# Kernel optimization log

Measured on AMD Instinct MI355X. Metric: run time of the kernel, lower is better.

The kernel has to match this reference:

```python
import jax, jax.numpy as jnp
import numpy as np

B, N1, N2, C1, C2, MLP_OUT = 16, 4096, 1024, 128, 256, 256


def setup_inputs() -> dict:
    key = jax.random.key(0)
    k = jax.random.split(key, 8)
    xyz1 = jax.random.normal(k[0], (B, N1, 3), dtype=jnp.float32)
    feat1 = jax.random.normal(k[1], (B, N1, C1), dtype=jnp.float32)
    xyz2 = jax.random.normal(k[2], (B, N2, 3), dtype=jnp.float32)
    feat2 = jax.random.normal(k[3], (B, N2, C2), dtype=jnp.float32)
    d_in = C1 + C2
    W1 = jax.random.normal(k[4], (d_in, MLP_OUT), dtype=jnp.float32) / np.sqrt(d_in)
    b1 = jnp.zeros((MLP_OUT,), dtype=jnp.float32)
    W2 = jax.random.normal(k[5], (MLP_OUT, MLP_OUT), dtype=jnp.float32) / np.sqrt(MLP_OUT)
    b2 = jnp.zeros((MLP_OUT,), dtype=jnp.float32)
    return {"xyz1": xyz1, "feat1": feat1, "xyz2": xyz2, "feat2": feat2,
            "W1": W1, "b1": b1, "W2": W2, "b2": b2}


def reference(xyz1, feat1, xyz2, feat2, W1, b1, W2, b2):
    # squared pairwise distances [B, N1, N2]
    dists = jnp.sum((xyz1[:, :, None, :] - xyz2[:, None, :, :]) ** 2, axis=-1)
    # 3 nearest neighbors (smallest distances)
    neg_d3, idx = jax.lax.top_k(-dists, 3)      # [B, N1, 3]
    d3 = jnp.maximum(-neg_d3, 1e-10)
    w = 1.0 / d3
    w = w / jnp.sum(w, axis=-1, keepdims=True)   # [B, N1, 3]
    # gather neighbor features: [B, N1, 3, C2]
    neighbor_feats = jax.vmap(lambda f, i: f[i])(feat2, idx)
    interpolated = jnp.sum(w[..., None] * neighbor_feats, axis=2)  # [B, N1, C2]
    new_feat = jnp.concatenate([interpolated, feat1], axis=-1)     # [B, N1, C2+C1]
    h = jax.nn.relu(new_feat @ W1 + b1)
    return jax.nn.relu(h @ W2 + b2)
```

## Files before the change

kernel.cpp:

```cpp
#include <hip/hip_runtime.h>
#include <cstdint>
#include <cstddef>

typedef unsigned short ushort_t;
typedef unsigned int uint_t;

typedef __bf16 bf16x8 __attribute__((ext_vector_type(8)));
typedef float floatx4 __attribute__((ext_vector_type(4)));

#define B_ 16
#define N1_ 4096
#define N2_ 1024
#define C1_ 128
#define C2_ 256
#define DIN_ 384
#define DOUT_ 256
#define M_ (B_ * N1_)


__device__ __forceinline__ ushort_t f2bf(float f) {
  unsigned int u = __builtin_bit_cast(unsigned int, f);
  u = (u + 0x7fffu + ((u >> 16) & 1u)) >> 16;
  return (ushort_t)u;
}


__global__ __launch_bounds__(256) void prep_kernel(
    const float* __restrict__ W1, const float* __restrict__ W2,
    ushort_t* __restrict__ W1s, ushort_t* __restrict__ W2s) {
  int e = blockIdx.x * 256 + threadIdx.x;
  if (e < DOUT_ * DIN_) {
    int kk = e & 31, n = (e >> 5) & 255, t = e >> 13;
    W1s[e] = f2bf(W1[(size_t)(t * 32 + kk) * DOUT_ + n]);
  }
  if (e < DOUT_ * DOUT_) {
    int kk = e & 31, n = (e >> 5) & 255, t = e >> 13;
    W2s[e] = f2bf(W2[(size_t)(t * 32 + kk) * DOUT_ + n]);
  }
}


__device__ __forceinline__ void ins_exact(float& s0, float& s1, float& s2,
                                          int& i0, int& i1, int& i2,
                                          float d, int p) {
  float ns2 = __builtin_amdgcn_fmed3f(d, s1, s2);
  float ns1 = __builtin_amdgcn_fmed3f(d, s0, s1);
  float ns0 = fminf(d, s0);
  bool c0 = d < s0, c1 = d < s1, c2 = d < s2;
  i2 = c1 ? i1 : (c2 ? p : i2);
  i1 = c0 ? i0 : (c1 ? p : i1);
  i0 = c0 ? p : i0;
  s0 = ns0; s1 = ns1; s2 = ns2;
}

__device__ __forceinline__ void ins_merge(float& s0, float& s1, float& s2,
                                          int& i0, int& i1, int& i2,
                                          float e, int j) {
  bool t0 = (e < s0) || (e == s0 && j < i0);
  bool t1 = (e < s1) || (e == s1 && j < i1);
  bool t2 = (e < s2) || (e == s2 && j < i2);
  s2 = t1 ? s1 : (t2 ? e : s2);
  i2 = t1 ? i1 : (t2 ? j : i2);
  s1 = t0 ? s0 : (t1 ? e : s1);
  i1 = t0 ? i0 : (t1 ? j : i1);
  s0 = t0 ? e : s0;
  i0 = t0 ? j : i0;
}


__global__ __launch_bounds__(256, 2) void fused_kernel(
    const float* __restrict__ xyz1, const float* __restrict__ xyz2,
    const float* __restrict__ feat1, const float* __restrict__ feat2,
    const ushort_t* __restrict__ W1s, const float* __restrict__ b1,
    const ushort_t* __restrict__ W2s, const float* __restrict__ b2,
    float* __restrict__ out) {
  __shared__ __align__(16) ushort_t As[32 * 384];
  __shared__ int idxL[32 * 3];
  __shared__ float wL[32 * 3];

  const int tid = threadIdx.x;
  const int wave = tid >> 6;
  const int lane = tid & 63;
  const int m = lane & 15;
  const int q = lane >> 4;
  const int row0 = blockIdx.x * 32;
  const int b = row0 >> 12;

  float4* xs4 = (float4*)As;
  {
    const float4* p24 = (const float4*)(xyz2 + (size_t)b * (N2_ * 3));
    float4 A = p24[3 * tid + 0];
    float4 Bv = p24[3 * tid + 1];
    float4 Cv = p24[3 * tid + 2];
    xs4[4 * tid + 0] = make_float4(A.x, A.y, A.z, 0.0f);
    xs4[4 * tid + 1] = make_float4(A.w, Bv.x, Bv.y, 0.0f);
    xs4[4 * tid + 2] = make_float4(Bv.z, Bv.w, Cv.x, 0.0f);
    xs4[4 * tid + 3] = make_float4(Cv.y, Cv.z, Cv.w, 0.0f);
  }
  __syncthreads();

  {
    const int g = tid >> 3;
    const int sub = tid & 7;
    const int row = row0 + g;
    const float* p1 = xyz1 + (size_t)row * 3;
    float x1 = p1[0], y1 = p1[1], z1 = p1[2];

    float s0 = 3.0e38f, s1 = 3.0e38f, s2 = 3.0e38f;
    int i0 = 0, i1 = 0, i2 = 0;

    int p = sub;
#pragma unroll 8
    for (int t = 0; t < N2_ / 8; ++t) {
      float4 qv = xs4[p];
      float dx = x1 - qv.x;
      float dy = y1 - qv.y;
      float dz = z1 - qv.z;
      float d = dx * dx + dy * dy + dz * dz;
      ins_exact(s0, s1, s2, i0, i1, i2, d, p);
      p += 8;
    }

#pragma unroll
    for (int mm = 1; mm <= 4; mm <<= 1) {
      float e0 = __shfl_xor(s0, mm), e1 = __shfl_xor(s1, mm), e2 = __shfl_xor(s2, mm);
      int j0 = __shfl_xor(i0, mm), j1 = __shfl_xor(i1, mm), j2 = __shfl_xor(i2, mm);
      ins_merge(s0, s1, s2, i0, i1, i2, e0, j0);
      ins_merge(s0, s1, s2, i0, i1, i2, e1, j1);
      ins_merge(s0, s1, s2, i0, i1, i2, e2, j2);
    }

    if (sub == 0) {
      float r0 = 1.0f / fmaxf(s0, 1e-10f);
      float r1 = 1.0f / fmaxf(s1, 1e-10f);
      float r2 = 1.0f / fmaxf(s2, 1e-10f);
      float s = 1.0f / (r0 + r1 + r2);
      idxL[g * 3 + 0] = i0;
      idxL[g * 3 + 1] = i1;
      idxL[g * 3 + 2] = i2;
      wL[g * 3 + 0] = r0 * s;
      wL[g * 3 + 1] = r1 * s;
      wL[g * 3 + 2] = r2 * s;
    }
  }
  __syncthreads();

#pragma unroll 4
  for (int it = 0; it < 8; ++it) {
    int rl = wave * 8 + it;
    int row = row0 + rl;
    int i0 = idxL[rl * 3 + 0], i1 = idxL[rl * 3 + 1], i2 = idxL[rl * 3 + 2];
    float w0 = wL[rl * 3 + 0], w1 = wL[rl * 3 + 1], w2 = wL[rl * 3 + 2];

    const float4* f0 = (const float4*)(feat2 + ((size_t)b * N2_ + i0) * C2_);
    const float4* f1 = (const float4*)(feat2 + ((size_t)b * N2_ + i1) * C2_);
    const float4* f2 = (const float4*)(feat2 + ((size_t)b * N2_ + i2) * C2_);
    float4 a = f0[lane];
    float4 c = f1[lane];
    float4 d = f2[lane];
    float vx = w0 * a.x + w1 * c.x + w2 * d.x;
    float vy = w0 * a.y + w1 * c.y + w2 * d.y;
    float vz = w0 * a.z + w1 * c.z + w2 * d.z;
    float vw = w0 * a.w + w1 * c.w + w2 * d.w;
    uint_t lo = (uint_t)f2bf(vx) | ((uint_t)f2bf(vy) << 16);
    uint_t hi = (uint_t)f2bf(vz) | ((uint_t)f2bf(vw) << 16);
    int e = (lane >> 3) * 1024 + rl * 32 + ((4 * lane) & 31);
    *(uint2*)&As[e] = make_uint2(lo, hi);

    float2 t1 = ((const float2*)(feat1 + (size_t)row * C1_))[lane];
    uint_t pk = (uint_t)f2bf(t1.x) | ((uint_t)f2bf(t1.y) << 16);
    int e1 = (8 + (lane >> 4)) * 1024 + rl * 32 + ((2 * lane) & 31);
    *(uint_t*)&As[e1] = pk;
  }
  __syncthreads();

  const int b_off = (wave * 64 + m) * 32 + q * 8;
  const int a_base = m * 32 + q * 8;

  floatx4 acc[2][4];
#pragma unroll
  for (int i = 0; i < 2; ++i)
#pragma unroll
    for (int j = 0; j < 4; ++j) acc[i][j] = (floatx4)0.0f;

  {
    bf16x8 bf0[4], bf1[4], af[2];
#pragma unroll
    for (int j = 0; j < 4; ++j)
      bf0[j] = *(const bf16x8*)(W1s + b_off + j * 512);
#pragma unroll
    for (int t = 0; t < 12; t += 2) {
#pragma unroll
      for (int j = 0; j < 4; ++j)
        bf1[j] = *(const bf16x8*)(W1s + (size_t)(t + 1) * 8192 + b_off + j * 512);
#pragma unroll
      for (int i = 0; i < 2; ++i)
        af[i] = *(const bf16x8*)&As[t * 1024 + a_base + i * 512];
#pragma unroll
      for (int i = 0; i < 2; ++i)
#pragma unroll
        for (int j = 0; j < 4; ++j)
          acc[i][j] = __builtin_amdgcn_mfma_f32_16x16x32_bf16(af[i], bf0[j],
                                                              acc[i][j], 0, 0, 0);
      if (t + 2 < 12) {
#pragma unroll
        for (int j = 0; j < 4; ++j)
          bf0[j] = *(const bf16x8*)(W1s + (size_t)(t + 2) * 8192 + b_off + j * 512);
      }
#pragma unroll
      for (int i = 0; i < 2; ++i)
        af[i] = *(const bf16x8*)&As[(t + 1) * 1024 + a_base + i * 512];
#pragma unroll
      for (int i = 0; i < 2; ++i)
#pragma unroll
        for (int j = 0; j < 4; ++j)
          acc[i][j] = __builtin_amdgcn_mfma_f32_16x16x32_bf16(af[i], bf1[j],
                                                              acc[i][j], 0, 0, 0);
    }
  }
  __syncthreads();

  ushort_t* HS = As;
#pragma unroll
  for (int j = 0; j < 4; ++j) {
    int col = wave * 64 + j * 16 + m;
    float bv = b1[col];
    int cb = (col >> 3) & 3;
    int tb = (col >> 5) * 1024 + (col & 7);
#pragma unroll
    for (int i = 0; i < 2; ++i)
#pragma unroll
      for (int r = 0; r < 4; ++r) {
        int row = i * 16 + q * 4 + r;
        float v = acc[i][j][r] + bv;
        v = v > 0.0f ? v : 0.0f;
        int ch = cb ^ ((row >> 2) & 3);
        HS[tb + row * 32 + ch * 8] = f2bf(v);
      }
  }
  __syncthreads();

  floatx4 acc2[2][4];
#pragma unroll
  for (int i = 0; i < 2; ++i)
#pragma unroll
    for (int j = 0; j < 4; ++j) acc2[i][j] = (floatx4)0.0f;

  {
    bf16x8 bf0[4], bf1[4], af[2];
#pragma unroll
    for (int j = 0; j < 4; ++j)
      bf0[j] = *(const bf16x8*)(W2s + b_off + j * 512);
#pragma unroll
    for (int t = 0; t < 8; t += 2) {
#pragma unroll
      for (int j = 0; j < 4; ++j)
        bf1[j] = *(const bf16x8*)(W2s + (size_t)(t + 1) * 8192 + b_off + j * 512);
#pragma unroll
      for (int i = 0; i < 2; ++i) {
        int row = m + 16 * i;
        int ch = q ^ ((row >> 2) & 3);
        af[i] = *(const bf16x8*)&HS[t * 1024 + row * 32 + ch * 8];
      }
#pragma unroll
      for (int i = 0; i < 2; ++i)
#pragma unroll
        for (int j = 0; j < 4; ++j)
          acc2[i][j] = __builtin_amdgcn_mfma_f32_16x16x32_bf16(af[i], bf0[j],
                                                               acc2[i][j], 0, 0, 0);
      if (t + 2 < 8) {
#pragma unroll
        for (int j = 0; j < 4; ++j)
          bf0[j] = *(const bf16x8*)(W2s + (size_t)(t + 2) * 8192 + b_off + j * 512);
      }
#pragma unroll
      for (int i = 0; i < 2; ++i) {
        int row = m + 16 * i;
        int ch = q ^ ((row >> 2) & 3);
        af[i] = *(const bf16x8*)&HS[(t + 1) * 1024 + row * 32 + ch * 8];
      }
#pragma unroll
      for (int i = 0; i < 2; ++i)
#pragma unroll
        for (int j = 0; j < 4; ++j)
          acc2[i][j] = __builtin_amdgcn_mfma_f32_16x16x32_bf16(af[i], bf1[j],
                                                               acc2[i][j], 0, 0, 0);
    }
  }

#pragma unroll
  for (int j = 0; j < 4; ++j) {
    int col = wave * 64 + j * 16 + m;
    float bv = b2[col];
#pragma unroll
    for (int i = 0; i < 2; ++i)
#pragma unroll
      for (int r = 0; r < 4; ++r) {
        int row = i * 16 + q * 4 + r;
        float v = acc2[i][j][r] + bv;
        v = v > 0.0f ? v : 0.0f;
        out[(size_t)(row0 + row) * DOUT_ + col] = v;
      }
  }
}


constexpr size_t OFF_W1S = 0;
constexpr size_t OFF_W2S = OFF_W1S + 196608;
constexpr size_t WS_TOTAL = OFF_W2S + 131072;

extern "C" void kernel_launch(void* const* d_in, const int* in_sizes, int n_in,
                              void* d_out, int out_size, void* d_ws, size_t ws_size,
                              hipStream_t stream) {
  const float* xyz1 = (const float*)d_in[0];
  const float* feat1 = (const float*)d_in[1];
  const float* xyz2 = (const float*)d_in[2];
  const float* feat2 = (const float*)d_in[3];
  const float* W1 = (const float*)d_in[4];
  const float* b1 = (const float*)d_in[5];
  const float* W2 = (const float*)d_in[6];
  const float* b2 = (const float*)d_in[7];

  if (ws_size < WS_TOTAL) return;

  char* ws = (char*)d_ws;
  ushort_t* W1s = (ushort_t*)(ws + OFF_W1S);
  ushort_t* W2s = (ushort_t*)(ws + OFF_W2S);

  prep_kernel<<<384, 256, 0, stream>>>(W1, W2, W1s, W2s);
  fused_kernel<<<M_ / 32, 256, 0, stream>>>(xyz1, xyz2, feat1, feat2, W1s, b1,
                                            W2s, b2, (float*)d_out);
}
```

Measured before the change: 182.0 us.

## Process two row tiles per block, interleaving next-tile KNN with current MFMA GEMMs

Each block now handles 64 rows as two 32-row sub-tiles. The KNN distance scan for the second sub-tile is split into chunks placed between the MFMA steps of the first sub-tile's two GEMMs, so VALU work can overlap matrix-core work. xyz2 now sits in its own shared buffer instead of aliasing As, and the block count halves. This adds about 16KB of LDS and extra live registers, which could lower occupancy below the launch bound of 2 blocks per CU.

```diff
diff --git a/kernel.cpp b/kernel.cpp
--- a/kernel.cpp
+++ b/kernel.cpp
@@ -74,6 +74,7 @@
     const ushort_t* __restrict__ W1s, const float* __restrict__ b1,
     const ushort_t* __restrict__ W2s, const float* __restrict__ b2,
     float* __restrict__ out) {
+  __shared__ __align__(16) float4 xs4[N2_];
   __shared__ __align__(16) ushort_t As[32 * 384];
   __shared__ int idxL[32 * 3];
   __shared__ float wL[32 * 3];
@@ -83,10 +84,9 @@
   const int lane = tid & 63;
   const int m = lane & 15;
   const int q = lane >> 4;
-  const int row0 = blockIdx.x * 32;
+  const int row0 = blockIdx.x * 64;
   const int b = row0 >> 12;
 
-  float4* xs4 = (float4*)As;
   {
     const float4* p24 = (const float4*)(xyz2 + (size_t)b * (N2_ * 3));
     float4 A = p24[3 * tid + 0];
@@ -99,28 +99,24 @@
   }
   __syncthreads();
 
+  const int gk = tid >> 3;
+  const int subk = tid & 7;
+
   {
-    const int g = tid >> 3;
-    const int sub = tid & 7;
-    const int row = row0 + g;
+    const int row = row0 + gk;
     const float* p1 = xyz1 + (size_t)row * 3;
     float x1 = p1[0], y1 = p1[1], z1 = p1[2];
-
     float s0 = 3.0e38f, s1 = 3.0e38f, s2 = 3.0e38f;
     int i0 = 0, i1 = 0, i2 = 0;
-
-    int p = sub;
+    int p = subk;
 #pragma unroll 8
     for (int t = 0; t < N2_ / 8; ++t) {
       float4 qv = xs4[p];
-      float dx = x1 - qv.x;
-      float dy = y1 - qv.y;
-      float dz = z1 - qv.z;
+      float dx = x1 - qv.x, dy = y1 - qv.y, dz = z1 - qv.z;
       float d = dx * dx + dy * dy + dz * dz;
       ins_exact(s0, s1, s2, i0, i1, i2, d, p);
       p += 8;
     }
-
 #pragma unroll
     for (int mm = 1; mm <= 4; mm <<= 1) {
       float e0 = __shfl_xor(s0, mm), e1 = __shfl_xor(s1, mm), e2 = __shfl_xor(s2, mm);
@@ -129,179 +125,222 @@
       ins_merge(s0, s1, s2, i0, i1, i2, e1, j1);
       ins_merge(s0, s1, s2, i0, i1, i2, e2, j2);
     }
-
-    if (sub == 0) {
+    if (subk == 0) {
       float r0 = 1.0f / fmaxf(s0, 1e-10f);
       float r1 = 1.0f / fmaxf(s1, 1e-10f);
       float r2 = 1.0f / fmaxf(s2, 1e-10f);
       float s = 1.0f / (r0 + r1 + r2);
-      idxL[g * 3 + 0] = i0;
-      idxL[g * 3 + 1] = i1;
-      idxL[g * 3 + 2] = i2;
-      wL[g * 3 + 0] = r0 * s;
-      wL[g * 3 + 1] = r1 * s;
-      wL[g * 3 + 2] = r2 * s;
+      idxL[gk * 3 + 0] = i0; idxL[gk * 3 + 1] = i1; idxL[gk * 3 + 2] = i2;
+      wL[gk * 3 + 0] = r0 * s; wL[gk * 3 + 1] = r1 * s; wL[gk * 3 + 2] = r2 * s;
     }
   }
   __syncthreads();
 
-#pragma unroll 4
-  for (int it = 0; it < 8; ++it) {
-    int rl = wave * 8 + it;
-    int row = row0 + rl;
-    int i0 = idxL[rl * 3 + 0], i1 = idxL[rl * 3 + 1], i2 = idxL[rl * 3 + 2];
-    float w0 = wL[rl * 3 + 0], w1 = wL[rl * 3 + 1], w2 = wL[rl * 3 + 2];
-
-    const float4* f0 = (const float4*)(feat2 + ((size_t)b * N2_ + i0) * C2_);
-    const float4* f1 = (const float4*)(feat2 + ((size_t)b * N2_ + i1) * C2_);
-    const float4* f2 = (const float4*)(feat2 + ((size_t)b * N2_ + i2) * C2_);
-    float4 a = f0[lane];
-    float4 c = f1[lane];
-    float4 d = f2[lane];
-    float vx = w0 * a.x + w1 * c.x + w2 * d.x;
-    float vy = w0 * a.y + w1 * c.y + w2 * d.y;
-    float vz = w0 * a.z + w1 * c.z + w2 * d.z;
-    float vw = w0 * a.w + w1 * c.w + w2 * d.w;
-    uint_t lo = (uint_t)f2bf(vx) | ((uint_t)f2bf(vy) << 16);
-    uint_t hi = (uint_t)f2bf(vz) | ((uint_t)f2bf(vw) << 16);
-    int e = (lane >> 3) * 1024 + rl * 32 + ((4 * lane) & 31);
-    *(uint2*)&As[e] = make_uint2(lo, hi);
-
-    float2 t1 = ((const float2*)(feat1 + (size_t)row * C1_))[lane];
-    uint_t pk = (uint_t)f2bf(t1.x) | ((uint_t)f2bf(t1.y) << 16);
-    int e1 = (8 + (lane >> 4)) * 1024 + rl * 32 + ((2 * lane) & 31);
-    *(uint_t*)&As[e1] = pk;
-  }
-  __syncthreads();
+  float kx, ky, kz;
+  float ks0 = 3.0e38f, ks1 = 3.0e38f, ks2 = 3.0e38f;
+  int ki0 = 0, ki1 = 0, ki2 = 0;
+  int pk = subk;
+  {
+    const float* p1 = xyz1 + (size_t)(row0 + 32 + gk) * 3;
+    kx = p1[0]; ky = p1[1]; kz = p1[2];
+  }
+
+#define KNN_CHUNK(N)                                                \
+  _Pragma("unroll") for (int cc_ = 0; cc_ < (N); ++cc_) {           \
+    float4 qv_ = xs4[pk];                                           \
+    float dx_ = kx - qv_.x, dy_ = ky - qv_.y, dz_ = kz - qv_.z;     \
+    float dd_ = dx_ * dx_ + dy_ * dy_ + dz_ * dz_;                  \
+    ins_exact(ks0, ks1, ks2, ki0, ki1, ki2, dd_, pk);               \
+    pk += 8;                                                        \
+  }
 
   const int b_off = (wave * 64 + m) * 32 + q * 8;
   const int a_base = m * 32 + q * 8;
 
-  floatx4 acc[2][4];
-#pragma unroll
-  for (int i = 0; i < 2; ++i)
-#pragma unroll
-    for (int j = 0; j < 4; ++j) acc[i][j] = (floatx4)0.0f;
-
-  {
-    bf16x8 bf0[4], bf1[4], af[2];
-#pragma unroll
-    for (int j = 0; j < 4; ++j)
-      bf0[j] = *(const bf16x8*)(W1s + b_off + j * 512);
-#pragma unroll
-    for (int t = 0; t < 12; t += 2) {
+  for (int st = 0; st < 2; ++st) {
+    const int row0t = row0 + st * 32;
+
+#pragma unroll 4
+    for (int it = 0; it < 8; ++it) {
+      int rl = wave * 8 + it;
+      int row = row0t + rl;
+      int i0 = idxL[rl * 3 + 0], i1 = idxL[rl * 3 + 1], i2 = idxL[rl * 3 + 2];
+      float w0 = wL[rl * 3 + 0], w1 = wL[rl * 3 + 1], w2 = wL[rl * 3 + 2];
+
+      const float4* f0 = (const float4*)(feat2 + ((size_t)b * N2_ + i0) * C2_);
+      const float4* f1 = (const float4*)(feat2 + ((size_t)b * N2_ + i1) * C2_);
+      const float4* f2 = (const float4*)(feat2 + ((size_t)b * N2_ + i2) * C2_);
+      float4 a = f0[lane];
+      float4 c = f1[lane];
+      float4 d = f2[lane];
+      float vx = w0 * a.x + w1 * c.x + w2 * d.x;
+      float vy = w0 * a.y + w1 * c.y + w2 * d.y;
+      float vz = w0 * a.z + w1 * c.z + w2 * d.z;
+      float vw = w0 * a.w + w1 * c.w + w2 * d.w;
+      uint_t lo = (uint_t)f2bf(vx) | ((uint_t)f2bf(vy) << 16);
+      uint_t hi = (uint_t)f2bf(vz) | ((uint_t)f2bf(vw) << 16);
+      int e = (lane >> 3) * 1024 + rl * 32 + ((4 * lane) & 31);
+      *(uint2*)&As[e] = make_uint2(lo, hi);
+
+      float2 t1 = ((const float2*)(feat1 + (size_t)row * C1_))[lane];
+      uint_t pkk = (uint_t)f2bf(t1.x) | ((uint_t)f2bf(t1.y) << 16);
+      int e1 = (8 + (lane >> 4)) * 1024 + rl * 32 + ((2 * lane) & 31);
+      *(uint_t*)&As[e1] = pkk;
+    }
+    __syncthreads();
+
+    floatx4 acc[2][4];
+#pragma unroll
+    for (int i = 0; i < 2; ++i)
+#pragma unroll
+      for (int j = 0; j < 4; ++j) acc[i][j] = (floatx4)0.0f;
+
+    {
+      bf16x8 bf0[4], bf1[4], af[2];
 #pragma unroll
       for (int j = 0; j < 4; ++j)
-        bf1[j] = *(const bf16x8*)(W1s + (size_t)(t + 1) * 8192 + b_off + j * 512);
+        bf0[j] = *(const bf16x8*)(W1s + b_off + j * 512);
+#pragma unroll
+      for (int t = 0; t < 12; t += 2) {
+#pragma unroll
+        for (int j = 0; j < 4; ++j)
+          bf1[j] = *(const bf16x8*)(W1s + (size_t)(t + 1) * 8192 + b_off + j * 512);
+#pragma unroll
+        for (int i = 0; i < 2; ++i)
+          af[i] = *(const bf16x8*)&As[t * 1024 + a_base + i * 512];
+#pragma unroll
+        for (int i = 0; i < 2; ++i)
+#pragma unroll
+          for (int j = 0; j < 4; ++j)
+            acc[i][j] = __builtin_amdgcn_mfma_f32_16x16x32_bf16(af[i], bf0[j],
+                                                                acc[i][j], 0, 0, 0);
+        if (st == 0) { KNN_CHUNK(6); }
+        if (t + 2 < 12) {
+#pragma unroll
+          for (int j = 0; j < 4; ++j)
+            bf0[j] = *(const bf16x8*)(W1s + (size_t)(t + 2) * 8192 + b_off + j * 512);
+        }
+#pragma unroll
+        for (int i = 0; i < 2; ++i)
+          af[i] = *(const bf16x8*)&As[(t + 1) * 1024 + a_base + i * 512];
+#pragma unroll
+        for (int i = 0; i < 2; ++i)
+#pragma unroll
+          for (int j = 0; j < 4; ++j)
+            acc[i][j] = __builtin_amdgcn_mfma_f32_16x16x32_bf16(af[i], bf1[j],
+                                                                acc[i][j], 0, 0, 0);
+        if (st == 0) { KNN_CHUNK(6); }
+      }
+    }
+    __syncthreads();
+
+    ushort_t* HS = As;
+#pragma unroll
+    for (int j = 0; j < 4; ++j) {
+      int col = wave * 64 + j * 16 + m;
+      float bv = b1[col];
+      int cb = (col >> 3) & 3;
+      int tb = (col >> 5) * 1024 + (col & 7);
 #pragma unroll
       for (int i = 0; i < 2; ++i)
-        af[i] = *(const bf16x8*)&As[t * 1024 + a_base + i * 512];
+#pragma unroll
+        for (int r = 0; r < 4; ++r) {
+          int row = i * 16 + q * 4 + r;
+          float v = acc[i][j][r] + bv;
+          v = v > 0.0f ? v : 0.0f;
+          int ch = cb ^ ((row >> 2) & 3);
+          HS[tb + row * 32 + ch * 8] = f2bf(v);
+        }
+    }
+    __syncthreads();
+
+    floatx4 acc2[2][4];
+#pragma unroll
+    for (int i = 0; i < 2; ++i)
+#pragma unroll
+      for (int j = 0; j < 4; ++j) acc2[i][j] = (floatx4)0.0f;
+
+    {
+      bf16x8 bf0[4], bf1[4], af[2];
+#pragma unroll
+      for (int j = 0; j < 4; ++j)
+        bf0[j] = *(const bf16x8*)(W2s + b_off + j * 512);
+#pragma unroll
+      for (int t = 0; t < 8; t += 2) {
+#pragma unroll
+        for (int j = 0; j < 4; ++j)
+          bf1[j] = *(const bf16x8*)(W2s + (size_t)(t + 1) * 8192 + b_off + j * 512);
+#pragma unroll
+        for (int i = 0; i < 2; ++i) {
+          int row = m + 16 * i;
+          int ch = q ^ ((row >> 2) & 3);
+          af[i] = *(const bf16x8*)&HS[t * 1024 + row * 32 + ch * 8];
+        }
+#pragma unroll
+        for (int i = 0; i < 2; ++i)
+#pragma unroll
+          for (int j = 0; j < 4; ++j)
+            acc2[i][j] = __builtin_amdgcn_mfma_f32_16x16x32_bf16(af[i], bf0[j],
+                                                                 acc2[i][j], 0, 0, 0);
+        if (st == 0) { KNN_CHUNK(6); }
+        if (t + 2 < 8) {
+#pragma unroll
+          for (int j = 0; j < 4; ++j)
+            bf0[j] = *(const bf16x8*)(W2s + (size_t)(t + 2) * 8192 + b_off + j * 512);
+        }
+#pragma unroll
+        for (int i = 0; i < 2; ++i) {
+          int row = m + 16 * i;
+          int ch = q ^ ((row >> 2) & 3);
+          af[i] = *(const bf16x8*)&HS[(t + 1) * 1024 + row * 32 + ch * 8];
+        }
+#pragma unroll
+        for (int i = 0; i < 2; ++i)
+#pragma unroll
+          for (int j = 0; j < 4; ++j)
+            acc2[i][j] = __builtin_amdgcn_mfma_f32_16x16x32_bf16(af[i], bf1[j],
+                                                                 acc2[i][j], 0, 0, 0);
+        if (st == 0) { KNN_CHUNK(6); }
+      }
+    }
+
+#pragma unroll
+    for (int j = 0; j < 4; ++j) {
+      int col = wave * 64 + j * 16 + m;
+      float bv = b2[col];
 #pragma unroll
       for (int i = 0; i < 2; ++i)
 #pragma unroll
-        for (int j = 0; j < 4; ++j)
-          acc[i][j] = __builtin_amdgcn_mfma_f32_16x16x32_bf16(af[i], bf0[j],
-                                                              acc[i][j], 0, 0, 0);
-      if (t + 2 < 12) {
-#pragma unroll
-        for (int j = 0; j < 4; ++j)
-          bf0[j] = *(const bf16x8*)(W1s + (size_t)(t + 2) * 8192 + b_off + j * 512);
+        for (int r = 0; r < 4; ++r) {
+          int row = i * 16 + q * 4 + r;
+          float v = acc2[i][j][r] + bv;
+          v = v > 0.0f ? v : 0.0f;
+          out[(size_t)(row0t + row) * DOUT_ + col] = v;
+        }
+    }
+
+    if (st == 0) {
+      KNN_CHUNK(8);
+#pragma unroll
+      for (int mm = 1; mm <= 4; mm <<= 1) {
+        float e0 = __shfl_xor(ks0, mm), e1 = __shfl_xor(ks1, mm), e2 = __shfl_xor(ks2, mm);
+        int j0 = __shfl_xor(ki0, mm), j1 = __shfl_xor(ki1, mm), j2 = __shfl_xor(ki2, mm);
+        ins_merge(ks0, ks1, ks2, ki0, ki1, ki2, e0, j0);
+        ins_merge(ks0, ks1, ks2, ki0, ki1, ki2, e1, j1);
+        ins_merge(ks0, ks1, ks2, ki0, ki1, ki2, e2, j2);
       }
-#pragma unroll
-      for (int i = 0; i < 2; ++i)
-        af[i] = *(const bf16x8*)&As[(t + 1) * 1024 + a_base + i * 512];
-#pragma unroll
-      for (int i = 0; i < 2; ++i)
-#pragma unroll
-        for (int j = 0; j < 4; ++j)
-          acc[i][j] = __builtin_amdgcn_mfma_f32_16x16x32_bf16(af[i], bf1[j],
-                                                              acc[i][j], 0, 0, 0);
-    }
-  }
-  __syncthreads();
-
-  ushort_t* HS = As;
-#pragma unroll
-  for (int j = 0; j < 4; ++j) {
-    int col = wave * 64 + j * 16 + m;
-    float bv = b1[col];
-    int cb = (col >> 3) & 3;
-    int tb = (col >> 5) * 1024 + (col & 7);
-#pragma unroll
-    for (int i = 0; i < 2; ++i)
-#pragma unroll
-      for (int r = 0; r < 4; ++r) {
-        int row = i * 16 + q * 4 + r;
-        float v = acc[i][j][r] + bv;
-        v = v > 0.0f ? v : 0.0f;
-        int ch = cb ^ ((row >> 2) & 3);
-        HS[tb + row * 32 + ch * 8] = f2bf(v);
+      if (subk == 0) {
+        float r0 = 1.0f / fmaxf(ks0, 1e-10f);
+        float r1 = 1.0f / fmaxf(ks1, 1e-10f);
+        float r2 = 1.0f / fmaxf(ks2, 1e-10f);
+        float s = 1.0f / (r0 + r1 + r2);
+        idxL[gk * 3 + 0] = ki0; idxL[gk * 3 + 1] = ki1; idxL[gk * 3 + 2] = ki2;
+        wL[gk * 3 + 0] = r0 * s; wL[gk * 3 + 1] = r1 * s; wL[gk * 3 + 2] = r2 * s;
       }
-  }
-  __syncthreads();
-
-  floatx4 acc2[2][4];
-#pragma unroll
-  for (int i = 0; i < 2; ++i)
-#pragma unroll
-    for (int j = 0; j < 4; ++j) acc2[i][j] = (floatx4)0.0f;
-
-  {
-    bf16x8 bf0[4], bf1[4], af[2];
-#pragma unroll
-    for (int j = 0; j < 4; ++j)
-      bf0[j] = *(const bf16x8*)(W2s + b_off + j * 512);
-#pragma unroll
-    for (int t = 0; t < 8; t += 2) {
-#pragma unroll
-      for (int j = 0; j < 4; ++j)
-        bf1[j] = *(const bf16x8*)(W2s + (size_t)(t + 1) * 8192 + b_off + j * 512);
-#pragma unroll
-      for (int i = 0; i < 2; ++i) {
-        int row = m + 16 * i;
-        int ch = q ^ ((row >> 2) & 3);
-        af[i] = *(const bf16x8*)&HS[t * 1024 + row * 32 + ch * 8];
-      }
-#pragma unroll
-      for (int i = 0; i < 2; ++i)
-#pragma unroll
-        for (int j = 0; j < 4; ++j)
-          acc2[i][j] = __builtin_amdgcn_mfma_f32_16x16x32_bf16(af[i], bf0[j],
-                                                               acc2[i][j], 0, 0, 0);
-      if (t + 2 < 8) {
-#pragma unroll
-        for (int j = 0; j < 4; ++j)
-          bf0[j] = *(const bf16x8*)(W2s + (size_t)(t + 2) * 8192 + b_off + j * 512);
-      }
-#pragma unroll
-      for (int i = 0; i < 2; ++i) {
-        int row = m + 16 * i;
-        int ch = q ^ ((row >> 2) & 3);
-        af[i] = *(const bf16x8*)&HS[(t + 1) * 1024 + row * 32 + ch * 8];
-      }
-#pragma unroll
-      for (int i = 0; i < 2; ++i)
-#pragma unroll
-        for (int j = 0; j < 4; ++j)
-          acc2[i][j] = __builtin_amdgcn_mfma_f32_16x16x32_bf16(af[i], bf1[j],
-                                                               acc2[i][j], 0, 0, 0);
-    }
-  }
-
-#pragma unroll
-  for (int j = 0; j < 4; ++j) {
-    int col = wave * 64 + j * 16 + m;
-    float bv = b2[col];
-#pragma unroll
-    for (int i = 0; i < 2; ++i)
-#pragma unroll
-      for (int r = 0; r < 4; ++r) {
-        int row = i * 16 + q * 4 + r;
-        float v = acc2[i][j][r] + bv;
-        v = v > 0.0f ? v : 0.0f;
-        out[(size_t)(row0 + row) * DOUT_ + col] = v;
-      }
-  }
+    }
+    __syncthreads();
+  }
+#undef KNN_CHUNK
 }
 
 
@@ -328,6 +367,6 @@
   ushort_t* W2s = (ushort_t*)(ws + OFF_W2S);
 
   prep_kernel<<<384, 256, 0, stream>>>(W1, W2, W1s, W2s);
-  fused_kernel<<<M_ / 32, 256, 0, stream>>>(xyz1, xyz2, feat1, feat2, W1s, b1,
+  fused_kernel<<<M_ / 64, 256, 0, stream>>>(xyz1, xyz2, feat1, feat2, W1s, b1,
                                             W2s, b2, (float*)d_out);
 }
```

New measurement: 367.6 us. 102% more time.

## Warp-specialize fused kernel: KNN crew overlaps next tile with MLP crew

Applied to the files above, without the earlier changes.

Doubles block size to 512 threads, splitting them into a KNN crew that computes nearest neighbors for the next 32-row tile and an MLP crew that gathers, interpolates and runs both MFMA GEMMs for the current tile. Each block now processes four tiles, double-buffering idx/weight arrays, and the xyz2 coordinates live in a dedicated shared buffer. The KNN loop is split into chunks between barriers, with two independent top-3 accumulators for ILP. The aim is to hide the scalar KNN scan behind matrix-core work. The cost is fewer blocks, idle threads in the final tile, and a fixed per-phase split of KNN iterations that may not match actual phase lengths.

```diff
diff --git a/kernel.cpp b/kernel.cpp
--- a/kernel.cpp
+++ b/kernel.cpp
@@ -16,6 +16,7 @@
 #define DIN_ 384
 #define DOUT_ 256
 #define M_ (B_ * N1_)
+#define TILES_ 4
 
 
 __device__ __forceinline__ ushort_t f2bf(float f) {
@@ -68,240 +69,289 @@
 }
 
 
-__global__ __launch_bounds__(256, 2) void fused_kernel(
+__global__ __launch_bounds__(512, 4) void fused_kernel(
     const float* __restrict__ xyz1, const float* __restrict__ xyz2,
     const float* __restrict__ feat1, const float* __restrict__ feat2,
     const ushort_t* __restrict__ W1s, const float* __restrict__ b1,
     const ushort_t* __restrict__ W2s, const float* __restrict__ b2,
     float* __restrict__ out) {
+  __shared__ __align__(16) float4 xs4[N2_];
   __shared__ __align__(16) ushort_t As[32 * 384];
-  __shared__ int idxL[32 * 3];
-  __shared__ float wL[32 * 3];
+  __shared__ int idxL[2][32 * 3];
+  __shared__ float wL[2][32 * 3];
 
   const int tid = threadIdx.x;
+  const int row0 = blockIdx.x * (TILES_ * 32);
+  const int b = row0 >> 12;
+
+  for (int i = tid; i < N2_; i += 512) {
+    const float* s = xyz2 + ((size_t)b * N2_ + i) * 3;
+    xs4[i] = make_float4(s[0], s[1], s[2], 0.0f);
+  }
+  __syncthreads();
+
+  const bool knnCrew = (tid >= 256);
+  const int kt = tid & 255;
+  const int gk = kt >> 3;
+  const int subk = kt & 7;
+
   const int wave = tid >> 6;
   const int lane = tid & 63;
   const int m = lane & 15;
   const int q = lane >> 4;
-  const int row0 = blockIdx.x * 32;
-  const int b = row0 >> 12;
-
-  float4* xs4 = (float4*)As;
-  {
-    const float4* p24 = (const float4*)(xyz2 + (size_t)b * (N2_ * 3));
-    float4 A = p24[3 * tid + 0];
-    float4 Bv = p24[3 * tid + 1];
-    float4 Cv = p24[3 * tid + 2];
-    xs4[4 * tid + 0] = make_float4(A.x, A.y, A.z, 0.0f);
-    xs4[4 * tid + 1] = make_float4(A.w, Bv.x, Bv.y, 0.0f);
-    xs4[4 * tid + 2] = make_float4(Bv.z, Bv.w, Cv.x, 0.0f);
-    xs4[4 * tid + 3] = make_float4(Cv.y, Cv.z, Cv.w, 0.0f);
-  }
-  __syncthreads();
-
-  {
-    const int g = tid >> 3;
-    const int sub = tid & 7;
-    const int row = row0 + g;
-    const float* p1 = xyz1 + (size_t)row * 3;
-    float x1 = p1[0], y1 = p1[1], z1 = p1[2];
-
-    float s0 = 3.0e38f, s1 = 3.0e38f, s2 = 3.0e38f;
-    int i0 = 0, i1 = 0, i2 = 0;
-
-    int p = sub;
-#pragma unroll 8
-    for (int t = 0; t < N2_ / 8; ++t) {
-      float4 qv = xs4[p];
-      float dx = x1 - qv.x;
-      float dy = y1 - qv.y;
-      float dz = z1 - qv.z;
-      float d = dx * dx + dy * dy + dz * dz;
-      ins_exact(s0, s1, s2, i0, i1, i2, d, p);
-      p += 8;
-    }
-
-#pragma unroll
-    for (int mm = 1; mm <= 4; mm <<= 1) {
-      float e0 = __shfl_xor(s0, mm), e1 = __shfl_xor(s1, mm), e2 = __shfl_xor(s2, mm);
-      int j0 = __shfl_xor(i0, mm), j1 = __shfl_xor(i1, mm), j2 = __shfl_xor(i2, mm);
-      ins_merge(s0, s1, s2, i0, i1, i2, e0, j0);
-      ins_merge(s0, s1, s2, i0, i1, i2, e1, j1);
-      ins_merge(s0, s1, s2, i0, i1, i2, e2, j2);
-    }
-
-    if (sub == 0) {
-      float r0 = 1.0f / fmaxf(s0, 1e-10f);
-      float r1 = 1.0f / fmaxf(s1, 1e-10f);
-      float r2 = 1.0f / fmaxf(s2, 1e-10f);
-      float s = 1.0f / (r0 + r1 + r2);
-      idxL[g * 3 + 0] = i0;
-      idxL[g * 3 + 1] = i1;
-      idxL[g * 3 + 2] = i2;
-      wL[g * 3 + 0] = r0 * s;
-      wL[g * 3 + 1] = r1 * s;
-      wL[g * 3 + 2] = r2 * s;
-    }
-  }
-  __syncthreads();
-
-#pragma unroll 4
-  for (int it = 0; it < 8; ++it) {
-    int rl = wave * 8 + it;
-    int row = row0 + rl;
-    int i0 = idxL[rl * 3 + 0], i1 = idxL[rl * 3 + 1], i2 = idxL[rl * 3 + 2];
-    float w0 = wL[rl * 3 + 0], w1 = wL[rl * 3 + 1], w2 = wL[rl * 3 + 2];
-
-    const float4* f0 = (const float4*)(feat2 + ((size_t)b * N2_ + i0) * C2_);
-    const float4* f1 = (const float4*)(feat2 + ((size_t)b * N2_ + i1) * C2_);
-    const float4* f2 = (const float4*)(feat2 + ((size_t)b * N2_ + i2) * C2_);
-    float4 a = f0[lane];
-    float4 c = f1[lane];
-    float4 d = f2[lane];
-    float vx = w0 * a.x + w1 * c.x + w2 * d.x;
-    float vy = w0 * a.y + w1 * c.y + w2 * d.y;
-    float vz = w0 * a.z + w1 * c.z + w2 * d.z;
-    float vw = w0 * a.w + w1 * c.w + w2 * d.w;
-    uint_t lo = (uint_t)f2bf(vx) | ((uint_t)f2bf(vy) << 16);
-    uint_t hi = (uint_t)f2bf(vz) | ((uint_t)f2bf(vw) << 16);
-    int e = (lane >> 3) * 1024 + rl * 32 + ((4 * lane) & 31);
-    *(uint2*)&As[e] = make_uint2(lo, hi);
-
-    float2 t1 = ((const float2*)(feat1 + (size_t)row * C1_))[lane];
-    uint_t pk = (uint_t)f2bf(t1.x) | ((uint_t)f2bf(t1.y) << 16);
-    int e1 = (8 + (lane >> 4)) * 1024 + rl * 32 + ((2 * lane) & 31);
-    *(uint_t*)&As[e1] = pk;
-  }
-  __syncthreads();
-
   const int b_off = (wave * 64 + m) * 32 + q * 8;
   const int a_base = m * 32 + q * 8;
 
-  floatx4 acc[2][4];
-#pragma unroll
-  for (int i = 0; i < 2; ++i)
-#pragma unroll
-    for (int j = 0; j < 4; ++j) acc[i][j] = (floatx4)0.0f;
-
-  {
-    bf16x8 bf0[4], bf1[4], af[2];
-#pragma unroll
-    for (int j = 0; j < 4; ++j)
-      bf0[j] = *(const bf16x8*)(W1s + b_off + j * 512);
-#pragma unroll
-    for (int t = 0; t < 12; t += 2) {
+  float kx, ky, kz;
+  float as0, as1, as2, bs0, bs1, bs2;
+  int ai0, ai1, ai2, bi0, bi1, bi2;
+  int pA, pB;
+
+#define KNN_INIT(ROW)                                   \
+  do {                                                  \
+    const float* p1_ = xyz1 + (size_t)(ROW) * 3;        \
+    kx = p1_[0]; ky = p1_[1]; kz = p1_[2];              \
+    as0 = 3.0e38f; as1 = 3.0e38f; as2 = 3.0e38f;        \
+    bs0 = 3.0e38f; bs1 = 3.0e38f; bs2 = 3.0e38f;        \
+    ai0 = 0; ai1 = 0; ai2 = 0;                          \
+    bi0 = 0; bi1 = 0; bi2 = 0;                          \
+    pA = subk; pB = subk + 8;                           \
+  } while (0)
+
+#define KNN_ITERS(N)                                              \
+  do {                                                            \
+    _Pragma("unroll 2") for (int ii_ = 0; ii_ < (N); ++ii_) {     \
+      float4 qa_ = xs4[pA];                                       \
+      float4 qb_ = xs4[pB];                                       \
+      {                                                           \
+        float dx_ = kx - qa_.x, dy_ = ky - qa_.y, dz_ = kz - qa_.z; \
+        float d_ = dx_ * dx_ + dy_ * dy_ + dz_ * dz_;             \
+        ins_exact(as0, as1, as2, ai0, ai1, ai2, d_, pA);          \
+      }                                                           \
+      {                                                           \
+        float dx_ = kx - qb_.x, dy_ = ky - qb_.y, dz_ = kz - qb_.z; \
+        float d_ = dx_ * dx_ + dy_ * dy_ + dz_ * dz_;             \
+        ins_exact(bs0, bs1, bs2, bi0, bi1, bi2, d_, pB);          \
+      }                                                           \
+      pA += 16; pB += 16;                                         \
+    }                                                             \
+  } while (0)
+
+#define KNN_FINISH(BUF)                                                     \
+  do {                                                                      \
+    ins_merge(as0, as1, as2, ai0, ai1, ai2, bs0, bi0);                      \
+    ins_merge(as0, as1, as2, ai0, ai1, ai2, bs1, bi1);                      \
+    ins_merge(as0, as1, as2, ai0, ai1, ai2, bs2, bi2);                      \
+    _Pragma("unroll") for (int mm_ = 1; mm_ <= 4; mm_ <<= 1) {              \
+      float e0_ = __shfl_xor(as0, mm_), e1_ = __shfl_xor(as1, mm_),         \
+            e2_ = __shfl_xor(as2, mm_);                                     \
+      int j0_ = __shfl_xor(ai0, mm_), j1_ = __shfl_xor(ai1, mm_),           \
+          j2_ = __shfl_xor(ai2, mm_);                                       \
+      ins_merge(as0, as1, as2, ai0, ai1, ai2, e0_, j0_);                    \
+      ins_merge(as0, as1, as2, ai0, ai1, ai2, e1_, j1_);                    \
+      ins_merge(as0, as1, as2, ai0, ai1, ai2, e2_, j2_);                    \
+    }                                                                       \
+    if (subk == 0) {                                                        \
+      float r0_ = 1.0f / fmaxf(as0, 1e-10f);                                \
+      float r1_ = 1.0f / fmaxf(as1, 1e-10f);                                \
+      float r2_ = 1.0f / fmaxf(as2, 1e-10f);                                \
+      float s_ = 1.0f / (r0_ + r1_ + r2_);                                  \
+      idxL[BUF][gk * 3 + 0] = ai0;                                          \
+      idxL[BUF][gk * 3 + 1] = ai1;                                          \
+      idxL[BUF][gk * 3 + 2] = ai2;                                          \
+      wL[BUF][gk * 3 + 0] = r0_ * s_;                                       \
+      wL[BUF][gk * 3 + 1] = r1_ * s_;                                       \
+      wL[BUF][gk * 3 + 2] = r2_ * s_;                                       \
+    }                                                                       \
+  } while (0)
+
+  if (knnCrew) {
+    KNN_INIT(row0 + gk);
+    KNN_ITERS(64);
+    KNN_FINISH(0);
+  }
+  __syncthreads();
+
+  for (int t = 0; t < TILES_; ++t) {
+    const int cur = t & 1;
+    const int row0t = row0 + t * 32;
+    const bool haveNext = (t + 1 < TILES_);
+
+    if (!knnCrew) {
+#pragma unroll 4
+      for (int it = 0; it < 8; ++it) {
+        int rl = wave * 8 + it;
+        int row = row0t + rl;
+        int i0 = idxL[cur][rl * 3 + 0], i1 = idxL[cur][rl * 3 + 1],
+            i2 = idxL[cur][rl * 3 + 2];
+        float w0 = wL[cur][rl * 3 + 0], w1 = wL[cur][rl * 3 + 1],
+              w2 = wL[cur][rl * 3 + 2];
+
+        const float4* f0 = (const float4*)(feat2 + ((size_t)b * N2_ + i0) * C2_);
+        const float4* f1 = (const float4*)(feat2 + ((size_t)b * N2_ + i1) * C2_);
+        const float4* f2 = (const float4*)(feat2 + ((size_t)b * N2_ + i2) * C2_);
+        float4 a = f0[lane];
+        float4 c = f1[lane];
+        float4 d = f2[lane];
+        float vx = w0 * a.x + w1 * c.x + w2 * d.x;
+        float vy = w0 * a.y + w1 * c.y + w2 * d.y;
+        float vz = w0 * a.z + w1 * c.z + w2 * d.z;
+        float vw = w0 * a.w + w1 * c.w + w2 * d.w;
+        uint_t lo = (uint_t)f2bf(vx) | ((uint_t)f2bf(vy) << 16);
+        uint_t hi = (uint_t)f2bf(vz) | ((uint_t)f2bf(vw) << 16);
+        int e = (lane >> 3) * 1024 + rl * 32 + ((4 * lane) & 31);
+        *(uint2*)&As[e] = make_uint2(lo, hi);
+
+        float2 t1 = ((const float2*)(feat1 + (size_t)row * C1_))[lane];
+        uint_t pkk = (uint_t)f2bf(t1.x) | ((uint_t)f2bf(t1.y) << 16);
+        int e1 = (8 + (lane >> 4)) * 1024 + rl * 32 + ((2 * lane) & 31);
+        *(uint_t*)&As[e1] = pkk;
+      }
+    } else if (haveNext) {
+      KNN_INIT(row0 + (t + 1) * 32 + gk);
+      KNN_ITERS(22);
+    }
+    __syncthreads();
+
+    floatx4 acc[2][4];
+    if (!knnCrew) {
+#pragma unroll
+      for (int i = 0; i < 2; ++i)
+#pragma unroll
+        for (int j = 0; j < 4; ++j) acc[i][j] = (floatx4)0.0f;
+
+      bf16x8 bf0[4], bf1[4], af[2];
 #pragma unroll
       for (int j = 0; j < 4; ++j)
-        bf1[j] = *(const bf16x8*)(W1s + (size_t)(t + 1) * 8192 + b_off + j * 512);
+        bf0[j] = *(const bf16x8*)(W1s + b_off + j * 512);
+#pragma unroll
+      for (int tt = 0; tt < 12; tt += 2) {
+#pragma unroll
+        for (int j = 0; j < 4; ++j)
+          bf1[j] = *(const bf16x8*)(W1s + (size_t)(tt + 1) * 8192 + b_off + j * 512);
+#pragma unroll
+        for (int i = 0; i < 2; ++i)
+          af[i] = *(const bf16x8*)&As[tt * 1024 + a_base + i * 512];
+#pragma unroll
+        for (int i = 0; i < 2; ++i)
+#pragma unroll
+          for (int j = 0; j < 4; ++j)
+            acc[i][j] = __builtin_amdgcn_mfma_f32_16x16x32_bf16(af[i], bf0[j],
+                                                                acc[i][j], 0, 0, 0);
+        if (tt + 2 < 12) {
+#pragma unroll
+          for (int j = 0; j < 4; ++j)
+            bf0[j] = *(const bf16x8*)(W1s + (size_t)(tt + 2) * 8192 + b_off + j * 512);
+        }
+#pragma unroll
+        for (int i = 0; i < 2; ++i)
+          af[i] = *(const bf16x8*)&As[(tt + 1) * 1024 + a_base + i * 512];
+#pragma unroll
+        for (int i = 0; i < 2; ++i)
+#pragma unroll
+          for (int j = 0; j < 4; ++j)
+            acc[i][j] = __builtin_amdgcn_mfma_f32_16x16x32_bf16(af[i], bf1[j],
+                                                                acc[i][j], 0, 0, 0);
+      }
+    } else if (haveNext) {
+      KNN_ITERS(22);
+    }
+    __syncthreads();
+
+    ushort_t* HS = As;
+    if (!knnCrew) {
+#pragma unroll
+      for (int j = 0; j < 4; ++j) {
+        int col = wave * 64 + j * 16 + m;
+        float bv = b1[col];
+        int cb = (col >> 3) & 3;
+        int tb = (col >> 5) * 1024 + (col & 7);
+#pragma unroll
+        for (int i = 0; i < 2; ++i)
+#pragma unroll
+          for (int r = 0; r < 4; ++r) {
+            int row = i * 16 + q * 4 + r;
+            float v = acc[i][j][r] + bv;
+            v = v > 0.0f ? v : 0.0f;
+            int ch = cb ^ ((row >> 2) & 3);
+            HS[tb + row * 32 + ch * 8] = f2bf(v);
+          }
+      }
+    } else if (haveNext) {
+      KNN_ITERS(10);
+    }
+    __syncthreads();
+
+    if (!knnCrew) {
+      floatx4 acc2[2][4];
 #pragma unroll
       for (int i = 0; i < 2; ++i)
-        af[i] = *(const bf16x8*)&As[t * 1024 + a_base + i * 512];
-#pragma unroll
-      for (int i = 0; i < 2; ++i)
+#pragma unroll
+        for (int j = 0; j < 4; ++j) acc2[i][j] = (floatx4)0.0f;
+
+      bf16x8 bf0[4], bf1[4], af[2];
+#pragma unroll
+      for (int j = 0; j < 4; ++j)
+        bf0[j] = *(const bf16x8*)(W2s + b_off + j * 512);
+#pragma unroll
+      for (int tt = 0; tt < 8; tt += 2) {
 #pragma unroll
         for (int j = 0; j < 4; ++j)
-          acc[i][j] = __builtin_amdgcn_mfma_f32_16x16x32_bf16(af[i], bf0[j],
-                                                              acc[i][j], 0, 0, 0);
-      if (t + 2 < 12) {
-#pragma unroll
-        for (int j = 0; j < 4; ++j)
-          bf0[j] = *(const bf16x8*)(W1s + (size_t)(t + 2) * 8192 + b_off + j * 512);
-      }
-#pragma unroll
-      for (int i = 0; i < 2; ++i)
-        af[i] = *(const bf16x8*)&As[(t + 1) * 1024 + a_base + i * 512];
-#pragma unroll
-      for (int i = 0; i < 2; ++i)
-#pragma unroll
-        for (int j = 0; j < 4; ++j)
-          acc[i][j] = __builtin_amdgcn_mfma_f32_16x16x32_bf16(af[i], bf1[j],
-                                                              acc[i][j], 0, 0, 0);
+          bf1[j] = *(const bf16x8*)(W2s + (size_t)(tt + 1) * 8192 + b_off + j * 512);
+#pragma unroll
+        for (int i = 0; i < 2; ++i) {
+          int row = m + 16 * i;
+          int ch = q ^ ((row >> 2) & 3);
+          af[i] = *(const bf16x8*)&HS[tt * 1024 + row * 32 + ch * 8];
+        }
+#pragma unroll
+        for (int i = 0; i < 2; ++i)
+#pragma unroll
+          for (int j = 0; j < 4; ++j)
+            acc2[i][j] = __builtin_amdgcn_mfma_f32_16x16x32_bf16(af[i], bf0[j],
+                                                                 acc2[i][j], 0, 0, 0);
+        if (tt + 2 < 8) {
+#pragma unroll
+          for (int j = 0; j < 4; ++j)
+            bf0[j] = *(const bf16x8*)(W2s + (size_t)(tt + 2) * 8192 + b_off + j * 512);
+        }
+#pragma unroll
+        for (int i = 0; i < 2; ++i) {
+          int row = m + 16 * i;
+          int ch = q ^ ((row >> 2) & 3);
+          af[i] = *(const bf16x8*)&HS[(tt + 1) * 1024 + row * 32 + ch * 8];
+        }
+#pragma unroll
+        for (int i = 0; i < 2; ++i)
+#pragma unroll
+          for (int j = 0; j < 4; ++j)
+            acc2[i][j] = __builtin_amdgcn_mfma_f32_16x16x32_bf16(af[i], bf1[j],
+                                                                 acc2[i][j], 0, 0, 0);
+      }
+
+#pragma unroll
+      for (int j = 0; j < 4; ++j) {
+        int col = wave * 64 + j * 16 + m;
+        float bv = b2[col];
+#pragma unroll
+        for (int i = 0; i < 2; ++i)
+#pragma unroll
+          for (int r = 0; r < 4; ++r) {
+            int row = i * 16 + q * 4 + r;
+            float v = acc2[i][j][r] + bv;
+            v = v > 0.0f ? v : 0.0f;
+            out[(size_t)(row0t + row) * DOUT_ + col] = v;
+          }
+      }
+    } else if (haveNext) {
+      KNN_ITERS(10);
+      KNN_FINISH(cur ^ 1);
     }
-  }
-  __syncthreads();
-
-  ushort_t* HS = As;
-#pragma unroll
-  for (int j = 0; j < 4; ++j) {
-    int col = wave * 64 + j * 16 + m;
-    float bv = b1[col];
-    int cb = (col >> 3) & 3;
-    int tb = (col >> 5) * 1024 + (col & 7);
-#pragma unroll
-    for (int i = 0; i < 2; ++i)
-#pragma unroll
-      for (int r = 0; r < 4; ++r) {
-        int row = i * 16 + q * 4 + r;
-        float v = acc[i][j][r] + bv;
-        v = v > 0.0f ? v : 0.0f;
-        int ch = cb ^ ((row >> 2) & 3);
-        HS[tb + row * 32 + ch * 8] = f2bf(v);
-      }
-  }
-  __syncthreads();
-
-  floatx4 acc2[2][4];
-#pragma unroll
-  for (int i = 0; i < 2; ++i)
-#pragma unroll
-    for (int j = 0; j < 4; ++j) acc2[i][j] = (floatx4)0.0f;
-
-  {
-    bf16x8 bf0[4], bf1[4], af[2];
-#pragma unroll
-    for (int j = 0; j < 4; ++j)
-      bf0[j] = *(const bf16x8*)(W2s + b_off + j * 512);
-#pragma unroll
-    for (int t = 0; t < 8; t += 2) {
-#pragma unroll
-      for (int j = 0; j < 4; ++j)
-        bf1[j] = *(const bf16x8*)(W2s + (size_t)(t + 1) * 8192 + b_off + j * 512);
-#pragma unroll
-      for (int i = 0; i < 2; ++i) {
-        int row = m + 16 * i;
-        int ch = q ^ ((row >> 2) & 3);
-        af[i] = *(const bf16x8*)&HS[t * 1024 + row * 32 + ch * 8];
-      }
-#pragma unroll
-      for (int i = 0; i < 2; ++i)
-#pragma unroll
-        for (int j = 0; j < 4; ++j)
-          acc2[i][j] = __builtin_amdgcn_mfma_f32_16x16x32_bf16(af[i], bf0[j],
-                                                               acc2[i][j], 0, 0, 0);
-      if (t + 2 < 8) {
-#pragma unroll
-        for (int j = 0; j < 4; ++j)
-          bf0[j] = *(const bf16x8*)(W2s + (size_t)(t + 2) * 8192 + b_off + j * 512);
-      }
-#pragma unroll
-      for (int i = 0; i < 2; ++i) {
-        int row = m + 16 * i;
-        int ch = q ^ ((row >> 2) & 3);
-        af[i] = *(const bf16x8*)&HS[(t + 1) * 1024 + row * 32 + ch * 8];
-      }
-#pragma unroll
-      for (int i = 0; i < 2; ++i)
-#pragma unroll
-        for (int j = 0; j < 4; ++j)
-          acc2[i][j] = __builtin_amdgcn_mfma_f32_16x16x32_bf16(af[i], bf1[j],
-                                                               acc2[i][j], 0, 0, 0);
-    }
-  }
-
-#pragma unroll
-  for (int j = 0; j < 4; ++j) {
-    int col = wave * 64 + j * 16 + m;
-    float bv = b2[col];
-#pragma unroll
-    for (int i = 0; i < 2; ++i)
-#pragma unroll
-      for (int r = 0; r < 4; ++r) {
-        int row = i * 16 + q * 4 + r;
-        float v = acc2[i][j][r] + bv;
-        v = v > 0.0f ? v : 0.0f;
-        out[(size_t)(row0 + row) * DOUT_ + col] = v;
-      }
-  }
+    __syncthreads();
+  }
+#undef KNN_INIT
+#undef KNN_ITERS
+#undef KNN_FINISH
 }
 
 
@@ -328,6 +378,6 @@
   ushort_t* W2s = (ushort_t*)(ws + OFF_W2S);
 
   prep_kernel<<<384, 256, 0, stream>>>(W1, W2, W1s, W2s);
-  fused_kernel<<<M_ / 32, 256, 0, stream>>>(xyz1, xyz2, feat1, feat2, W1s, b1,
-                                            W2s, b2, (float*)d_out);
-}
+  fused_kernel<<<M_ / (TILES_ * 32), 512, 0, stream>>>(
+      xyz1, xyz2, feat1, feat2, W1s, b1, W2s, b2, (float*)d_out);
+}
```

Result: slower. 325.4 us (+78.8%).
